# Kernel optimization log

Measured on AMD Instinct MI355X. Metric: run time of the kernel, lower is better.

## Reference

```python
import jax, jax.numpy as jnp
import numpy as np

D_MODEL = 1024
N_HEADS = 16
D_HEAD = D_MODEL // N_HEADS
B, T = 4, 2048


def setup_inputs() -> dict:
    key = jax.random.key(0)
    ks = jax.random.split(key, 9)
    s = 0.02
    return {
        "x": jax.random.normal(ks[0], (B, T, D_MODEL), dtype=jnp.float32),
        "Wq": jax.random.normal(ks[1], (D_MODEL, D_MODEL), dtype=jnp.float32) * s,
        "bq": jnp.zeros((D_MODEL,), dtype=jnp.float32),
        "Wk": jax.random.normal(ks[2], (D_MODEL, D_MODEL), dtype=jnp.float32) * s,
        "bk": jnp.zeros((D_MODEL,), dtype=jnp.float32),
        "Wv": jax.random.normal(ks[3], (D_MODEL, D_MODEL), dtype=jnp.float32) * s,
        "bv": jnp.zeros((D_MODEL,), dtype=jnp.float32),
        "Wo": jax.random.normal(ks[4], (D_MODEL, D_MODEL), dtype=jnp.float32) * s,
        "bo": jnp.zeros((D_MODEL,), dtype=jnp.float32),
    }


def reference(x, Wq, bq, Wk, bk, Wv, bv, Wo, bo):
    # Dropout in eval mode (identity), as standard for a correctness baseline.
    Bx, Tx, _ = x.shape
    # torch nn.Linear: y = x @ W.T + b
    Q = x @ Wq.T + bq
    K = x @ Wk.T + bk
    V = x @ Wv.T + bv
    # [B, T, H, Dh] -> [B, H, T, Dh]
    Q = Q.reshape(Bx, Tx, N_HEADS, D_HEAD).transpose(0, 2, 1, 3)
    K = K.reshape(Bx, Tx, N_HEADS, D_HEAD).transpose(0, 2, 1, 3)
    V = V.reshape(Bx, Tx, N_HEADS, D_HEAD).transpose(0, 2, 1, 3)
    scale = 1.0 / jnp.sqrt(jnp.float32(D_HEAD))
    scores = jnp.einsum("bhqd,bhkd->bhqk", Q, K) * scale  # [B,H,T,T]
    # additive causal mask: -1e6 above the diagonal (matches torch.triu trick)
    mask = jnp.triu(jnp.full((Tx, Tx), -1000000.0, dtype=scores.dtype), k=1)
    scores = scores + mask
    attn = jax.nn.softmax(scores, axis=-1)
    out = jnp.einsum("bhqk,bhkd->bhqd", attn, V)  # [B,H,T,Dh]
    out = out.transpose(0, 2, 1, 3).reshape(Bx, Tx, D_MODEL)
    out = out @ Wo.T + bo
    return out
```

## Files before the change

kernel.cpp:

```cpp
#include <hip/hip_runtime.h>
#include <stdint.h>

#define DM 1024
#define HEADS 16
#define DH 64
#define BQ 4
#define TT 2048
#define MTOT (BQ*TT)
#define NQT (TT/64)

typedef __attribute__((ext_vector_type(8))) __bf16 bf16x8;
typedef __attribute__((ext_vector_type(4))) float f32x4;
typedef __attribute__((ext_vector_type(4))) uint32_t u32x4;
typedef unsigned short u16;
typedef __attribute__((ext_vector_type(8))) unsigned short u16x8;

__device__ __forceinline__ u16 f2b(float f) {
  uint32_t u = __builtin_bit_cast(uint32_t, f);
  u = (u + 0x7fffu + ((u >> 16) & 1u)) >> 16;
  return (u16)u;
}

__device__ __forceinline__ uint32_t cvtpk(float lo, float hi) {
  uint32_t r;
  asm("v_cvt_pk_bf16_f32 %0, %1, %2" : "=v"(r) : "v"(lo), "v"(hi));
  return r;
}

__device__ __forceinline__ void gload_lds16(const u16* g, u16* l) {
  __builtin_amdgcn_global_load_lds(
      (const __attribute__((address_space(1))) void*)g,
      (__attribute__((address_space(3))) void*)l, 16, 0, 0);
}

#define NX (MTOT * DM / 4)
#define NW (DM * DM / 4)
__global__ __launch_bounds__(256) void cast_all(const float* __restrict__ x,
                                                const float* __restrict__ Wq,
                                                const float* __restrict__ Wk,
                                                const float* __restrict__ Wv,
                                                const float* __restrict__ Wo,
                                                u16* __restrict__ xb,
                                                u16* __restrict__ wqkvb,
                                                u16* __restrict__ wob) {
  int i = blockIdx.x * 256 + threadIdx.x;
  const float* src; u16* dst;
  if (i < NX)               { src = x;  dst = xb; }
  else if (i < NX + NW)     { src = Wq; dst = wqkvb;          i -= NX; }
  else if (i < NX + 2 * NW) { src = Wk; dst = wqkvb + 4 * NW; i -= NX + NW; }
  else if (i < NX + 3 * NW) { src = Wv; dst = wqkvb + 8 * NW; i -= NX + 2 * NW; }
  else                      { src = Wo; dst = wob;            i -= NX + 3 * NW; }
  float4 v = ((const float4*)src)[i];
  ushort4 o;
  o.x = f2b(v.x); o.y = f2b(v.y); o.z = f2b(v.z); o.w = f2b(v.w);
  ((ushort4*)dst)[i] = o;
}

#define SLOT_QA (256 * 32)
#define SLOT_QB (128 * 32)
#define SLOT_QE (SLOT_QA + SLOT_QB)

__global__ __launch_bounds__(512, 2) void gemm_qkv8(const u16* __restrict__ A,
                                                    const u16* __restrict__ W,
                                                    const float* __restrict__ bq,
                                                    const float* __restrict__ bk,
                                                    const float* __restrict__ bv,
                                                    u16* __restrict__ Qo,
                                                    u16* __restrict__ Ko,
                                                    u16* __restrict__ Vto,
                                                    float qs) {
  __shared__ u16 lds[4 * SLOT_QE];
  const int tid = threadIdx.x, lane = tid & 63, wave = tid >> 6;
  const int fr = lane & 15, g = lane >> 4;
  const int wm = wave >> 1, wn = wave & 1;

  int bid = blockIdx.x;
  bid = (bid & 7) * 96 + (bid >> 3);
  const int by = bid / 24, bx = bid % 24;
  const int m0 = by * 256, n0 = bx * 128;

  const int srow = tid >> 2;
  const int schunk = (tid & 3) ^ ((tid >> 3) & 3);
  const u16* gA0 = A + (size_t)(m0 + srow) * DM + schunk * 8;
  const u16* gA1 = gA0 + (size_t)128 * DM;
  const u16* gB0 = W + (size_t)(n0 + srow) * DM + schunk * 8;
  const int dA0 = wave * 512;
  const int dA1 = 4096 + wave * 512;
  const int dB0 = SLOT_QA + wave * 512;

#define STAGEQ(slot, kt) {                                   \
    u16* ls = &lds[(slot) * SLOT_QE];                        \
    const int ke = (kt) * 32;                                \
    gload_lds16(gA0 + ke, ls + dA0);                         \
    gload_lds16(gA1 + ke, ls + dA1);                         \
    gload_lds16(gB0 + ke, ls + dB0); }

  const int rchunk = (g ^ ((fr >> 1) & 3)) * 8;
  const int offA = (wm * 64 + fr) * 32 + rchunk;
  const int offB = SLOT_QA + (wn * 64 + fr) * 32 + rchunk;

  f32x4 acc[4][4];
#pragma unroll
  for (int mi = 0; mi < 4; ++mi)
#pragma unroll
    for (int ni = 0; ni < 4; ++ni) acc[mi][ni] = (f32x4){0.f, 0.f, 0.f, 0.f};

  bf16x8 afA[4], bfA[4], afB[4], bfB[4];

#define READQ(AFv, BFv, kt) {                                \
    const u16* sl = &lds[((kt) & 3) * SLOT_QE];              \
    _Pragma("unroll")                                        \
    for (int mi = 0; mi < 4; ++mi)                           \
      AFv[mi] = *(const bf16x8*)&sl[offA + mi * 512];        \
    _Pragma("unroll")                                        \
    for (int ni = 0; ni < 4; ++ni)                           \
      BFv[ni] = *(const bf16x8*)&sl[offB + ni * 512]; }

#define MFMAQ(AFv, BFv) {                                    \
    __builtin_amdgcn_s_setprio(1);                           \
    _Pragma("unroll")                                        \
    for (int mi = 0; mi < 4; ++mi)                           \
      _Pragma("unroll")                                      \
      for (int ni = 0; ni < 4; ++ni)                         \
        acc[mi][ni] = __builtin_amdgcn_mfma_f32_16x16x32_bf16(AFv[mi], BFv[ni], acc[mi][ni], 0, 0, 0); \
    __builtin_amdgcn_s_setprio(0); }

#define QW3 asm volatile("s_waitcnt vmcnt(3)" ::: "memory"); \
            asm volatile("s_barrier" ::: "memory");
#define QW0 asm volatile("s_waitcnt vmcnt(0)" ::: "memory"); \
            asm volatile("s_barrier" ::: "memory");

  STAGEQ(0, 0)
  STAGEQ(1, 1)
  STAGEQ(2, 2)
  asm volatile("s_waitcnt vmcnt(6)" ::: "memory");
  asm volatile("s_barrier" ::: "memory");
  READQ(afA, bfA, 0)

  for (int kt = 0; kt < 28; kt += 2) {
    QW3
    READQ(afB, bfB, kt + 1)
    MFMAQ(afA, bfA)
    STAGEQ((kt + 3) & 3, kt + 3)
    QW3
    READQ(afA, bfA, kt + 2)
    MFMAQ(afB, bfB)
    STAGEQ((kt + 4) & 3, kt + 4)
  }
  QW3
  READQ(afB, bfB, 29)
  MFMAQ(afA, bfA)
  STAGEQ(3, 31)
  QW3
  READQ(afA, bfA, 30)
  MFMAQ(afB, bfB)
  QW0
  READQ(afB, bfB, 31)
  MFMAQ(afA, bfA)
  MFMAQ(afB, bfB)

  const int g4 = g * 4;
  const int seg = n0 >> 10;
  const int nbase = (n0 & 1023) + wn * 64 + fr;
  if (seg == 0) {
#pragma unroll
    for (int ni = 0; ni < 4; ++ni) {
      const int cgl = nbase + ni * 16;
      const float bb = bq[cgl];
      const int hh = cgl >> 6, d = cgl & 63;
#pragma unroll
      for (int mi = 0; mi < 4; ++mi) {
        const int m = m0 + wm * 64 + mi * 16 + g4;
        const int bi = m >> 11, t = m & 2047;
        u16* dst = &Qo[(((size_t)bi * HEADS + hh) * TT + t) * DH + d];
#pragma unroll
        for (int j = 0; j < 4; ++j)
          dst[(size_t)j * DH] = f2b((acc[mi][ni][j] + bb) * qs);
      }
    }
  } else if (seg == 1) {
#pragma unroll
    for (int ni = 0; ni < 4; ++ni) {
      const int cgl = nbase + ni * 16;
      const float bb = bk[cgl];
      const int hh = cgl >> 6, d = cgl & 63;
#pragma unroll
      for (int mi = 0; mi < 4; ++mi) {
        const int m = m0 + wm * 64 + mi * 16 + g4;
        const int bi = m >> 11, t = m & 2047;
        u16* dst = &Ko[(((size_t)bi * HEADS + hh) * TT + t) * DH + d];
#pragma unroll
        for (int j = 0; j < 4; ++j)
          dst[(size_t)j * DH] = f2b(acc[mi][ni][j] + bb);
      }
    }
  } else {
#pragma unroll
    for (int ni = 0; ni < 4; ++ni) {
      const int cgl = nbase + ni * 16;
      const float bb = bv[cgl];
      const int hh = cgl >> 6, d = cgl & 63;
#pragma unroll
      for (int mi = 0; mi < 4; ++mi) {
        const int m = m0 + wm * 64 + mi * 16 + g4;
        const int t0 = m & 2047, bi = m >> 11;
        const int w64 = t0 & 63;
        const int pos = (t0 & ~63) | (((w64 >> 5) & 1) << 5) | (((w64 >> 2) & 3) << 3) |
                        (((w64 >> 4) & 1) << 2);
        ushort4 o;
        o.x = f2b(acc[mi][ni][0] + bb);
        o.y = f2b(acc[mi][ni][1] + bb);
        o.z = f2b(acc[mi][ni][2] + bb);
        o.w = f2b(acc[mi][ni][3] + bb);
        *(ushort4*)&Vto[(((size_t)bi * HEADS + hh) * DH + d) * TT + pos] = o;
      }
    }
  }
#undef STAGEQ
#undef READQ
#undef MFMAQ
#undef QW3
#undef QW0
}

#define SLOT_OA (256 * 32)
#define SLOT_OB (128 * 32)
#define SLOT_OE (SLOT_OA + SLOT_OB)

__global__ __launch_bounds__(512, 2) void gemm_out8(const u16* __restrict__ A,
                                                    const u16* __restrict__ Bw,
                                                    const float* __restrict__ bias,
                                                    float* __restrict__ outp) {
  __shared__ u16 lds[4 * SLOT_OE];
  const int tid = threadIdx.x, lane = tid & 63, wave = tid >> 6;
  const int fr = lane & 15, g = lane >> 4;
  const int wm = wave >> 1, wn = wave & 1;

  const int bx = blockIdx.x >> 5, by = blockIdx.x & 31;
  const int m0 = by * 256, n0 = bx * 128;

  const int srow = tid >> 2;
  const int schunk = (tid & 3) ^ ((tid >> 3) & 3);
  const u16* gA0 = A + (size_t)(m0 + srow) * DM + schunk * 8;
  const u16* gA1 = gA0 + (size_t)128 * DM;
  const u16* gB0 = Bw + (size_t)(n0 + srow) * DM + schunk * 8;
  const int dA0 = wave * 512;
  const int dA1 = 4096 + wave * 512;
  const int dB0 = SLOT_OA + wave * 512;

#define STAGEO(slot, kt) {                                   \
    u16* ls = &lds[(slot) * SLOT_OE];                        \
    const int ke = (kt) * 32;                                \
    gload_lds16(gA0 + ke, ls + dA0);                         \
    gload_lds16(gA1 + ke, ls + dA1);                         \
    gload_lds16(gB0 + ke, ls + dB0); }

  const int rchunk = (g ^ ((fr >> 1) & 3)) * 8;
  const int offA = (wm * 64 + fr) * 32 + rchunk;
  const int offB = SLOT_OA + (wn * 64 + fr) * 32 + rchunk;

  f32x4 acc[4][4];
#pragma unroll
  for (int mi = 0; mi < 4; ++mi)
#pragma unroll
    for (int ni = 0; ni < 4; ++ni) acc[mi][ni] = (f32x4){0.f, 0.f, 0.f, 0.f};

  bf16x8 afA[4], bfA[4], afB[4], bfB[4];

#define READO(AFv, BFv, kt) {                                \
    const u16* sl = &lds[((kt) & 3) * SLOT_OE];              \
    _Pragma("unroll")                                        \
    for (int mi = 0; mi < 4; ++mi)                           \
      AFv[mi] = *(const bf16x8*)&sl[offA + mi * 512];        \
    _Pragma("unroll")                                        \
    for (int ni = 0; ni < 4; ++ni)                           \
      BFv[ni] = *(const bf16x8*)&sl[offB + ni * 512]; }

#define MFMAO(AFv, BFv) {                                    \
    __builtin_amdgcn_s_setprio(1);                           \
    _Pragma("unroll")                                        \
    for (int mi = 0; mi < 4; ++mi)                           \
      _Pragma("unroll")                                      \
      for (int ni = 0; ni < 4; ++ni)                         \
        acc[mi][ni] = __builtin_amdgcn_mfma_f32_16x16x32_bf16(AFv[mi], BFv[ni], acc[mi][ni], 0, 0, 0); \
    __builtin_amdgcn_s_setprio(0); }

#define OW3 asm volatile("s_waitcnt vmcnt(3)" ::: "memory"); \
            asm volatile("s_barrier" ::: "memory");
#define OW0 asm volatile("s_waitcnt vmcnt(0)" ::: "memory"); \
            asm volatile("s_barrier" ::: "memory");

  STAGEO(0, 0)
  STAGEO(1, 1)
  STAGEO(2, 2)
  asm volatile("s_waitcnt vmcnt(6)" ::: "memory");
  asm volatile("s_barrier" ::: "memory");
  READO(afA, bfA, 0)

  for (int kt = 0; kt < 28; kt += 2) {
    OW3
    READO(afB, bfB, kt + 1)
    MFMAO(afA, bfA)
    STAGEO((kt + 3) & 3, kt + 3)
    OW3
    READO(afA, bfA, kt + 2)
    MFMAO(afB, bfB)
    STAGEO((kt + 4) & 3, kt + 4)
  }
  OW3
  READO(afB, bfB, 29)
  MFMAO(afA, bfA)
  STAGEO(3, 31)
  OW3
  READO(afA, bfA, 30)
  MFMAO(afB, bfB)
  OW0
  READO(afB, bfB, 31)
  MFMAO(afA, bfA)
  MFMAO(afB, bfB)

  const int g4 = g * 4;
#pragma unroll
  for (int mi = 0; mi < 4; ++mi) {
    const int rg = m0 + wm * 64 + mi * 16 + g4;
#pragma unroll
    for (int ni = 0; ni < 4; ++ni) {
      const int cg = n0 + wn * 64 + ni * 16 + fr;
      const float bb = bias[cg];
#pragma unroll
      for (int j = 0; j < 4; ++j)
        outp[(size_t)(rg + j) * DM + cg] = acc[mi][ni][j] + bb;
    }
  }
#undef STAGEO
#undef READO
#undef MFMAO
#undef OW3
#undef OW0
}

__global__ __launch_bounds__(256) void attn_fwd(const u16* __restrict__ Q,
                                                const u16* __restrict__ K,
                                                const u16* __restrict__ Vt,
                                                u16* __restrict__ O) {
  const int o_ = blockIdx.x;
  const int xcd = o_ & 7, j = o_ >> 3;
  const int gi = j & 7;
  const int qt128 = 15 - (j >> 3);
  const int gidx = xcd * 8 + gi;
  const int b = gidx >> 4, h = gidx & 15;
  const int tid = threadIdx.x, lane = tid & 63, wave = tid >> 6;
  __shared__ u16 Ks[64 * 64];
  __shared__ u16 Vs[64 * 64];

  const size_t bh = ((size_t)b * HEADS + h) * TT;
  const size_t vbse = ((size_t)b * HEADS + h) * DH;
  const int fr = lane & 15, g = lane >> 4;
  const int sr = tid >> 2;
  const int sc0 = tid & 3;

  const int sw1 = (sc0 ^ (sr & 7)) * 8;
  const int sw2 = ((sc0 + 4) ^ (sr & 7)) * 8;
  const int sgc = sc0 * 8;
  const int rk0 = (g ^ (fr & 7)) * 8;
  const int rk1 = ((4 + g) ^ (fr & 7)) * 8;
  const int k8 = g * 8;

  const int q0 = qt128 * 128;
  const int qtL = 2 * qt128, qtH = qtL + 1;
  const int qrowL = q0 + wave * 16 + fr;
  const int qrowH = q0 + 64 + wave * 16 + fr;
  const bf16x8 qfL0 = *(const bf16x8*)&Q[(bh + qrowL) * DH + k8];
  const bf16x8 qfL1 = *(const bf16x8*)&Q[(bh + qrowL) * DH + 32 + k8];
  const bf16x8 qfH0 = *(const bf16x8*)&Q[(bh + qrowH) * DH + k8];
  const bf16x8 qfH1 = *(const bf16x8*)&Q[(bh + qrowH) * DH + 32 + k8];

  float lsumL = 0.f, lsumH = 0.f;
  f32x4 oaccL[4], oaccH[4];
#pragma unroll
  for (int c = 0; c < 4; ++c) {
    oaccL[c] = (f32x4){0.f, 0.f, 0.f, 0.f};
    oaccH[c] = (f32x4){0.f, 0.f, 0.f, 0.f};
  }

  for (int kvb = 0; kvb <= qtH; ++kvb) {
    const int kv0 = kvb * 64;
    {
      const u16* kg = &K[(bh + kv0 + sr) * DH + sgc];
      u16x8 ka = *(const u16x8*)kg;
      u16x8 kc = *(const u16x8*)(kg + 32);
      const u16* vg = &Vt[(vbse + sr) * TT + kv0 + sgc];
      u16x8 va = *(const u16x8*)vg;
      u16x8 vc = *(const u16x8*)(vg + 32);
      *(u16x8*)&Ks[sr * 64 + sw1] = ka;
      *(u16x8*)&Ks[sr * 64 + sw2] = kc;
      *(u16x8*)&Vs[sr * 64 + sw1] = va;
      *(u16x8*)&Vs[sr * 64 + sw2] = vc;
    }
    __syncthreads();

    f32x4 sL[4], sH[4];
    __builtin_amdgcn_s_setprio(1);
#pragma unroll
    for (int c = 0; c < 4; ++c) {
      bf16x8 kb0 = *(const bf16x8*)&Ks[(c * 16 + fr) * 64 + rk0];
      bf16x8 kb1 = *(const bf16x8*)&Ks[(c * 16 + fr) * 64 + rk1];
      f32x4 tL = (f32x4){0.f, 0.f, 0.f, 0.f};
      tL = __builtin_amdgcn_mfma_f32_16x16x32_bf16(kb0, qfL0, tL, 0, 0, 0);
      tL = __builtin_amdgcn_mfma_f32_16x16x32_bf16(kb1, qfL1, tL, 0, 0, 0);
      sL[c] = tL;
      f32x4 tH = (f32x4){0.f, 0.f, 0.f, 0.f};
      tH = __builtin_amdgcn_mfma_f32_16x16x32_bf16(kb0, qfH0, tH, 0, 0, 0);
      tH = __builtin_amdgcn_mfma_f32_16x16x32_bf16(kb1, qfH1, tH, 0, 0, 0);
      sH[c] = tH;
    }
    __builtin_amdgcn_s_setprio(0);

    if (kvb >= qtL) {
#pragma unroll
      for (int c = 0; c < 4; ++c) {
        const int colg = kv0 + c * 16 + 4 * g;
#pragma unroll
        for (int r = 0; r < 4; ++r) {
          if (colg + r > qrowL) sL[c][r] = -1e30f;
          if (colg + r > qrowH) sH[c][r] = -1e30f;
        }
      }
    }

    float rsL = 0.f, rsH = 0.f;
    uint32_t pkL[8], pkH[8];
#pragma unroll
    for (int c = 0; c < 4; ++c) {
      float l0 = __builtin_amdgcn_exp2f(sL[c][0]);
      float l1 = __builtin_amdgcn_exp2f(sL[c][1]);
      float l2 = __builtin_amdgcn_exp2f(sL[c][2]);
      float l3 = __builtin_amdgcn_exp2f(sL[c][3]);
      rsL += (l0 + l1) + (l2 + l3);
      pkL[2 * c] = cvtpk(l0, l1);
      pkL[2 * c + 1] = cvtpk(l2, l3);
      float h0 = __builtin_amdgcn_exp2f(sH[c][0]);
      float h1 = __builtin_amdgcn_exp2f(sH[c][1]);
      float h2 = __builtin_amdgcn_exp2f(sH[c][2]);
      float h3 = __builtin_amdgcn_exp2f(sH[c][3]);
      rsH += (h0 + h1) + (h2 + h3);
      pkH[2 * c] = cvtpk(h0, h1);
      pkH[2 * c + 1] = cvtpk(h2, h3);
    }
    rsL += __shfl_xor(rsL, 16);
    rsL += __shfl_xor(rsL, 32);
    lsumL += rsL;
    rsH += __shfl_xor(rsH, 16);
    rsH += __shfl_xor(rsH, 32);
    lsumH += rsH;

    const bf16x8 paL0 = __builtin_bit_cast(bf16x8, (u32x4){pkL[0], pkL[1], pkL[2], pkL[3]});
    const bf16x8 paL1 = __builtin_bit_cast(bf16x8, (u32x4){pkL[4], pkL[5], pkL[6], pkL[7]});
    const bf16x8 paH0 = __builtin_bit_cast(bf16x8, (u32x4){pkH[0], pkH[1], pkH[2], pkH[3]});
    const bf16x8 paH1 = __builtin_bit_cast(bf16x8, (u32x4){pkH[4], pkH[5], pkH[6], pkH[7]});

    __builtin_amdgcn_s_setprio(1);
#pragma unroll
    for (int c = 0; c < 4; ++c) {
      bf16x8 vb0 = *(const bf16x8*)&Vs[(c * 16 + fr) * 64 + rk0];
      bf16x8 vb1 = *(const bf16x8*)&Vs[(c * 16 + fr) * 64 + rk1];
      oaccL[c] = __builtin_amdgcn_mfma_f32_16x16x32_bf16(vb0, paL0, oaccL[c], 0, 0, 0);
      oaccL[c] = __builtin_amdgcn_mfma_f32_16x16x32_bf16(vb1, paL1, oaccL[c], 0, 0, 0);
      oaccH[c] = __builtin_amdgcn_mfma_f32_16x16x32_bf16(vb0, paH0, oaccH[c], 0, 0, 0);
      oaccH[c] = __builtin_amdgcn_mfma_f32_16x16x32_bf16(vb1, paH1, oaccH[c], 0, 0, 0);
    }
    __builtin_amdgcn_s_setprio(0);
    __syncthreads();
  }

  const float invL = 1.f / lsumL;
#pragma unroll
  for (int c = 0; c < 4; ++c) {
    ushort4 o;
    o.x = f2b(oaccL[c][0] * invL);
    o.y = f2b(oaccL[c][1] * invL);
    o.z = f2b(oaccL[c][2] * invL);
    o.w = f2b(oaccL[c][3] * invL);
    *(ushort4*)&O[((size_t)b * TT + qrowL) * DM + h * DH + c * 16 + 4 * g] = o;
  }
  const float invH = 1.f / lsumH;
#pragma unroll
  for (int c = 0; c < 4; ++c) {
    ushort4 o;
    o.x = f2b(oaccH[c][0] * invH);
    o.y = f2b(oaccH[c][1] * invH);
    o.z = f2b(oaccH[c][2] * invH);
    o.w = f2b(oaccH[c][3] * invH);
    *(ushort4*)&O[((size_t)b * TT + qrowH) * DM + h * DH + c * 16 + 4 * g] = o;
  }
}

extern "C" void kernel_launch(void* const* d_in, const int* in_sizes, int n_in,
                              void* d_out, int out_size, void* d_ws, size_t ws_size,
                              hipStream_t stream) {
  const float* x  = (const float*)d_in[0];
  const float* Wq = (const float*)d_in[1];
  const float* bq = (const float*)d_in[2];
  const float* Wk = (const float*)d_in[3];
  const float* bk = (const float*)d_in[4];
  const float* Wv = (const float*)d_in[5];
  const float* bv = (const float*)d_in[6];
  const float* Wo = (const float*)d_in[7];
  const float* bo = (const float*)d_in[8];

  char* w = (char*)d_ws;
  u16* xb    = (u16*)w; w += (size_t)MTOT * DM * 2;
  u16* Wqkvb = (u16*)w; w += (size_t)3 * DM * DM * 2;
  u16* Wob   = (u16*)w; w += (size_t)DM * DM * 2;
  u16* Qb    = (u16*)w; w += (size_t)MTOT * DM * 2;
  u16* Kb    = (u16*)w; w += (size_t)MTOT * DM * 2;
  u16* Vtb   = (u16*)w; w += (size_t)MTOT * DM * 2;
  u16* AOb   = (u16*)w; w += (size_t)MTOT * DM * 2;

  cast_all<<<(NX + 4 * NW) / 256, 256, 0, stream>>>(x, Wq, Wk, Wv, Wo, xb, Wqkvb, Wob);

  const float qs = 0.125f * 1.44269504f;
  gemm_qkv8<<<768, 512, 0, stream>>>(xb, Wqkvb, bq, bk, bv, Qb, Kb, Vtb, qs);

  attn_fwd<<<1024, 256, 0, stream>>>(Qb, Kb, Vtb, AOb);

  gemm_out8<<<256, 512, 0, stream>>>(AOb, Wob, bo, (float*)d_out);
}
```

Measured before the change: 155.5 us.

## Double QKV GEMM K-tile to 64 with rotating triple-buffered LDS

The QKV projection GEMM now loads 64-wide K slices per stage instead of 32, halving the number of pipeline iterations and barriers. The fixed 4-slot ring is replaced by three pointer-rotated LDS buffers, with an XOR swizzle widened for 64-element rows. Each stage issues six async global-to-LDS loads and the wait count rises to match. The larger tiles roughly raise LDS use to about 147KB per block and double the fragment registers. That may stop two blocks from fitting per CU and raises register pressure.

```diff
diff --git a/kernel.cpp b/kernel.cpp
--- a/kernel.cpp
+++ b/kernel.cpp
@@ -56,9 +56,10 @@
   ((ushort4*)dst)[i] = o;
 }
 
-#define SLOT_QA (256 * 32)
-#define SLOT_QB (128 * 32)
-#define SLOT_QE (SLOT_QA + SLOT_QB)
+#define NK2 16
+#define SLOT_A2 (256 * 64)
+#define SLOT_B2 (128 * 64)
+#define SLOT_E2 (SLOT_A2 + SLOT_B2)
 
 __global__ __launch_bounds__(512, 2) void gemm_qkv8(const u16* __restrict__ A,
                                                     const u16* __restrict__ W,
@@ -69,7 +70,7 @@
                                                     u16* __restrict__ Ko,
                                                     u16* __restrict__ Vto,
                                                     float qs) {
-  __shared__ u16 lds[4 * SLOT_QE];
+  __shared__ u16 lds[3 * SLOT_E2];
   const int tid = threadIdx.x, lane = tid & 63, wave = tid >> 6;
   const int fr = lane & 15, g = lane >> 4;
   const int wm = wave >> 1, wn = wave & 1;
@@ -79,25 +80,26 @@
   const int by = bid / 24, bx = bid % 24;
   const int m0 = by * 256, n0 = bx * 128;
 
-  const int srow = tid >> 2;
-  const int schunk = (tid & 3) ^ ((tid >> 3) & 3);
-  const u16* gA0 = A + (size_t)(m0 + srow) * DM + schunk * 8;
-  const u16* gA1 = gA0 + (size_t)128 * DM;
-  const u16* gB0 = W + (size_t)(n0 + srow) * DM + schunk * 8;
+  const int lr8 = lane >> 3;
+  const int lsc = ((lane & 7) ^ lr8) * 8;
+  const u16* gA0 = A + (size_t)(m0 + wave * 8 + lr8) * DM + lsc;
+  const u16* gB0 = W + (size_t)(n0 + wave * 8 + lr8) * DM + lsc;
   const int dA0 = wave * 512;
-  const int dA1 = 4096 + wave * 512;
-  const int dB0 = SLOT_QA + wave * 512;
-
-#define STAGEQ(slot, kt) {                                   \
-    u16* ls = &lds[(slot) * SLOT_QE];                        \
-    const int ke = (kt) * 32;                                \
-    gload_lds16(gA0 + ke, ls + dA0);                         \
-    gload_lds16(gA1 + ke, ls + dA1);                         \
-    gload_lds16(gB0 + ke, ls + dB0); }
-
-  const int rchunk = (g ^ ((fr >> 1) & 3)) * 8;
-  const int offA = (wm * 64 + fr) * 32 + rchunk;
-  const int offB = SLOT_QA + (wn * 64 + fr) * 32 + rchunk;
+  const int dB0 = SLOT_A2 + wave * 512;
+
+#define STAGEQ(ls, kt) {                                     \
+    const int ke = (kt) * 64;                                \
+    gload_lds16(gA0 + ke,                (ls) + dA0);        \
+    gload_lds16(gA0 + ke + (size_t)64  * DM, (ls) + dA0 + 4096);  \
+    gload_lds16(gA0 + ke + (size_t)128 * DM, (ls) + dA0 + 8192);  \
+    gload_lds16(gA0 + ke + (size_t)192 * DM, (ls) + dA0 + 12288); \
+    gload_lds16(gB0 + ke,                (ls) + dB0);        \
+    gload_lds16(gB0 + ke + (size_t)64  * DM, (ls) + dB0 + 4096); }
+
+  const int rc0 = ((g) ^ (fr & 7)) * 8;
+  const int rc1 = ((4 + g) ^ (fr & 7)) * 8;
+  const int offA = (wm * 64 + fr) * 64;
+  const int offB = SLOT_A2 + (wn * 64 + fr) * 64;
 
   f32x4 acc[4][4];
 #pragma unroll
@@ -105,57 +107,61 @@
 #pragma unroll
     for (int ni = 0; ni < 4; ++ni) acc[mi][ni] = (f32x4){0.f, 0.f, 0.f, 0.f};
 
-  bf16x8 afA[4], bfA[4], afB[4], bfB[4];
-
-#define READQ(AFv, BFv, kt) {                                \
-    const u16* sl = &lds[((kt) & 3) * SLOT_QE];              \
+  bf16x8 afA[8], bfA[8], afB[8], bfB[8];
+
+#define READQ(AFv, BFv, ls) {                                \
     _Pragma("unroll")                                        \
-    for (int mi = 0; mi < 4; ++mi)                           \
-      AFv[mi] = *(const bf16x8*)&sl[offA + mi * 512];        \
+    for (int mi = 0; mi < 4; ++mi) {                         \
+      AFv[2 * mi]     = *(const bf16x8*)&(ls)[offA + mi * 1024 + rc0]; \
+      AFv[2 * mi + 1] = *(const bf16x8*)&(ls)[offA + mi * 1024 + rc1]; \
+    }                                                        \
     _Pragma("unroll")                                        \
-    for (int ni = 0; ni < 4; ++ni)                           \
-      BFv[ni] = *(const bf16x8*)&sl[offB + ni * 512]; }
+    for (int ni = 0; ni < 4; ++ni) {                         \
+      BFv[2 * ni]     = *(const bf16x8*)&(ls)[offB + ni * 1024 + rc0]; \
+      BFv[2 * ni + 1] = *(const bf16x8*)&(ls)[offB + ni * 1024 + rc1]; \
+    } }
 
 #define MFMAQ(AFv, BFv) {                                    \
     __builtin_amdgcn_s_setprio(1);                           \
     _Pragma("unroll")                                        \
     for (int mi = 0; mi < 4; ++mi)                           \
       _Pragma("unroll")                                      \
-      for (int ni = 0; ni < 4; ++ni)                         \
-        acc[mi][ni] = __builtin_amdgcn_mfma_f32_16x16x32_bf16(AFv[mi], BFv[ni], acc[mi][ni], 0, 0, 0); \
+      for (int ni = 0; ni < 4; ++ni) {                       \
+        acc[mi][ni] = __builtin_amdgcn_mfma_f32_16x16x32_bf16(AFv[2 * mi], BFv[2 * ni], acc[mi][ni], 0, 0, 0); \
+        acc[mi][ni] = __builtin_amdgcn_mfma_f32_16x16x32_bf16(AFv[2 * mi + 1], BFv[2 * ni + 1], acc[mi][ni], 0, 0, 0); \
+      }                                                      \
     __builtin_amdgcn_s_setprio(0); }
 
-#define QW3 asm volatile("s_waitcnt vmcnt(3)" ::: "memory"); \
+#define QW6 asm volatile("s_waitcnt vmcnt(6)" ::: "memory"); \
             asm volatile("s_barrier" ::: "memory");
 #define QW0 asm volatile("s_waitcnt vmcnt(0)" ::: "memory"); \
             asm volatile("s_barrier" ::: "memory");
 
-  STAGEQ(0, 0)
-  STAGEQ(1, 1)
-  STAGEQ(2, 2)
+  u16* p0 = &lds[0];
+  u16* p1 = &lds[SLOT_E2];
+  u16* p2 = &lds[2 * SLOT_E2];
+  u16 *pCur = p0, *pNxt = p1, *pStg = p2;
+
+  STAGEQ(p0, 0)
+  STAGEQ(p1, 1)
   asm volatile("s_waitcnt vmcnt(6)" ::: "memory");
   asm volatile("s_barrier" ::: "memory");
-  READQ(afA, bfA, 0)
-
-  for (int kt = 0; kt < 28; kt += 2) {
-    QW3
-    READQ(afB, bfB, kt + 1)
+  READQ(afA, bfA, p0)
+
+  for (int kt = 0; kt < NK2 - 2; kt += 2) {
+    STAGEQ(pStg, kt + 2)
+    QW6
+    READQ(afB, bfB, pNxt)
     MFMAQ(afA, bfA)
-    STAGEQ((kt + 3) & 3, kt + 3)
-    QW3
-    READQ(afA, bfA, kt + 2)
+    { u16* t = pCur; pCur = pNxt; pNxt = pStg; pStg = t; }
+    if (kt + 3 < NK2) { STAGEQ(pStg, kt + 3) }
+    QW6
+    READQ(afA, bfA, pNxt)
     MFMAQ(afB, bfB)
-    STAGEQ((kt + 4) & 3, kt + 4)
-  }
-  QW3
-  READQ(afB, bfB, 29)
-  MFMAQ(afA, bfA)
-  STAGEQ(3, 31)
-  QW3
-  READQ(afA, bfA, 30)
-  MFMAQ(afB, bfB)
+    { u16* t = pCur; pCur = pNxt; pNxt = pStg; pStg = t; }
+  }
   QW0
-  READQ(afB, bfB, 31)
+  READQ(afB, bfB, pNxt)
   MFMAQ(afA, bfA)
   MFMAQ(afB, bfB)
 
@@ -219,7 +225,7 @@
 #undef STAGEQ
 #undef READQ
 #undef MFMAQ
-#undef QW3
+#undef QW6
 #undef QW0
 }
 
```

After: 155.6 us. About the same (+0.0%).
